# Optimization experiments

Hardware: AMD Instinct MI355X
Metric: run time of the kernel (lower is better)

## Reference

```python
import jax, jax.numpy as jnp
import numpy as np

MIN_STDDEV = 1e-05
STATE, ACTION, HIDDEN, RNN_H = 32, 8, 32, 32
B, T = 16384, 64


def setup_inputs() -> dict:
    key = jax.random.key(0)
    ks = jax.random.split(key, 16)
    sc = 0.1
    return {
        "s0": jax.random.normal(ks[0], (B, STATE), jnp.float32),
        "h0": jax.random.normal(ks[1], (1, B, RNN_H), jnp.float32),
        "actions": jax.random.normal(ks[2], (B, T, ACTION), jnp.float32),
        # Elman RNN params (PyTorch layout: W_ih [H, S+A], W_hh [H, H])
        "W_ih": jax.random.normal(ks[3], (RNN_H, STATE + ACTION), jnp.float32) * sc,
        "W_hh": jax.random.normal(ks[4], (RNN_H, RNN_H), jnp.float32) * sc,
        "b_ih": jax.random.normal(ks[5], (RNN_H,), jnp.float32) * sc,
        "b_hh": jax.random.normal(ks[6], (RNN_H,), jnp.float32) * sc,
        # Transition MLP: h -> elu(fc1) -> (mean, stddev)
        "fc1_w": jax.random.normal(ks[7], (HIDDEN, RNN_H), jnp.float32) * sc,
        "fc1_b": jax.random.normal(ks[8], (HIDDEN,), jnp.float32) * sc,
        "mean_w": jax.random.normal(ks[9], (STATE, HIDDEN), jnp.float32) * sc,
        "mean_b": jax.random.normal(ks[10], (STATE,), jnp.float32) * sc,
        "std_w": jax.random.normal(ks[11], (STATE, HIDDEN), jnp.float32) * sc,
        "std_b": jax.random.normal(ks[12], (STATE,), jnp.float32) * sc,
        "horizon_length": T,
    }


def reference(s0, h0, actions, W_ih, W_hh, b_ih, b_hh, fc1_w, fc1_b,
              mean_w, mean_b, std_w, std_b, horizon_length):
    # RSSM.rollout with mean_only=True: per step
    #   h_t = tanh(W_ih @ [s_{t-1}, a_{t-1}] + b_ih + W_hh @ h_{t-1} + b_hh)
    #   prior_t = Transition(h_t): mean, stddev = MLP(h_t); sample = mean
    n_steps = min(int(horizon_length), actions.shape[1])
    acts = jnp.transpose(actions[:, :n_steps], (1, 0, 2))  # [T, B, A]

    def step(carry, a):
        h, s = carry  # h: [B, H], s: [B, STATE] (prior sample = mean)
        x = jnp.concatenate([s, a], axis=-1)  # [B, STATE+A]
        h = jnp.tanh(x @ W_ih.T + b_ih + h @ W_hh.T + b_hh)
        hid = jax.nn.elu(h @ fc1_w.T + fc1_b)
        mean = hid @ mean_w.T + mean_b
        stddev = jax.nn.softplus(hid @ std_w.T + std_b) + MIN_STDDEV
        return (h, mean), (mean, stddev)

    (_, _), (means, stddevs) = jax.lax.scan(step, (h0[0], s0), acts)
    # pack prior means and stddevs: [T, B, 2*STATE]
    return jnp.concatenate([means, stddevs], axis=-1)
```

## Files before the change

### kernel.cpp

```cpp
#include <hip/hip_runtime.h>


#define NBATCH 16384
#define NSTEP  64
#define U_STRIDE 72
#define HID_STRIDE 40

typedef short bf16x8 __attribute__((ext_vector_type(8)));
typedef float f32x4  __attribute__((ext_vector_type(4)));

__device__ __forceinline__ short f2bf(float f) {
    union { float f; unsigned int u; } c; c.f = f;
    unsigned int r = c.u + 0x7fffu + ((c.u >> 16) & 1u);
    return (short)(r >> 16);
}

__global__ __launch_bounds__(64) void rssm_kernel(
    const float* __restrict__ s0, const float* __restrict__ h0,
    const float* __restrict__ actions,
    const float* __restrict__ W_ih, const float* __restrict__ W_hh,
    const float* __restrict__ b_ih, const float* __restrict__ b_hh,
    const float* __restrict__ fc1_w, const float* __restrict__ fc1_b,
    const float* __restrict__ mean_w, const float* __restrict__ mean_b,
    const float* __restrict__ std_w, const float* __restrict__ std_b,
    float* __restrict__ out)
{
    __shared__ alignas(16) short u_lds[16 * U_STRIDE];
    __shared__ alignas(16) short act_lds[NSTEP * 16 * 8];
    __shared__ alignas(16) short hid_lds[16 * HID_STRIDE];

    const int lane = threadIdx.x;
    const int n    = lane & 15;
    const int q    = lane >> 4;
    const int base = blockIdx.x * 16;

    bf16x8 wb[2][3], fw[2], mw[2], sw[2];
    #pragma unroll
    for (int hf = 0; hf < 2; ++hf) {
        const int col = hf * 16 + n;
        #pragma unroll
        for (int c = 0; c < 3; ++c)
            #pragma unroll
            for (int j = 0; j < 8; ++j) {
                const int kk = q * 8 + j;
                float w = 0.f;
                if (c == 0)              w = W_ih[col * 40 + kk];
                else if (c == 1)         w = W_hh[col * 32 + kk];
                else if (kk < 8)         w = W_ih[col * 40 + 32 + kk];
                wb[hf][c][j] = f2bf(w);
            }
        #pragma unroll
        for (int j = 0; j < 8; ++j) {
            const int k = q * 8 + j;
            fw[hf][j] = f2bf(fc1_w [col * 32 + k]);
            mw[hf][j] = f2bf(mean_w[col * 32 + k]);
            sw[hf][j] = f2bf(std_w [col * 32 + k]);
        }
    }
    float bc[2], fb[2], mb[2], sb[2];
    #pragma unroll
    for (int hf = 0; hf < 2; ++hf) {
        const int col = hf * 16 + n;
        bc[hf] = b_ih[col] + b_hh[col];
        fb[hf] = fc1_b[col];
        mb[hf] = mean_b[col];
        sb[hf] = std_b[col];
    }

    {
        const int m = lane >> 2;
        const int k = (lane & 3) * 8;
        bf16x8 sv, hv;
        #pragma unroll
        for (int j = 0; j < 8; ++j) {
            sv[j] = f2bf(s0[(size_t)(base + m) * 32 + k + j]);
            hv[j] = f2bf(h0[(size_t)(base + m) * 32 + k + j]);
        }
        *(bf16x8*)(&u_lds[m * U_STRIDE + k]) = sv;
        *(bf16x8*)(&u_lds[m * U_STRIDE + 32 + k]) = hv;
    }

    {
        const int arow = lane & 15;
        const int aq   = lane >> 4;
        const float* ap = actions + (size_t)(base + arow) * (NSTEP * 8);
        #pragma unroll
        for (int tt = 0; tt < 16; ++tt) {
            const int t = tt * 4 + aq;
            const f32x4 lo = *(const f32x4*)(ap + t * 8);
            const f32x4 hi = *(const f32x4*)(ap + t * 8 + 4);
            bf16x8 av;
            #pragma unroll
            for (int j = 0; j < 4; ++j) { av[j] = f2bf(lo[j]); av[4 + j] = f2bf(hi[j]); }
            *(bf16x8*)(&act_lds[(t * 16 + arow) * 8]) = av;
        }
    }
    __builtin_amdgcn_wave_barrier();

    float* outp[4];
    #pragma unroll
    for (int r = 0; r < 4; ++r)
        outp[r] = out + (size_t)(base + q * 4 + r) * 64 + n;

    const bf16x8 zfrag = {0, 0, 0, 0, 0, 0, 0, 0};

    for (int t = 0; t < NSTEP; ++t) {
        bf16x8 ua0 = *(const bf16x8*)(&u_lds[n * U_STRIDE + q * 8]);
        bf16x8 ua1 = *(const bf16x8*)(&u_lds[n * U_STRIDE + 32 + q * 8]);
        bf16x8 af  = zfrag;
        if (q == 0) af = *(const bf16x8*)(&act_lds[(t * 16 + n) * 8]);

        f32x4 acc0 = {bc[0], bc[0], bc[0], bc[0]};
        f32x4 acc1 = {bc[1], bc[1], bc[1], bc[1]};
        acc0 = __builtin_amdgcn_mfma_f32_16x16x32_bf16(ua0, wb[0][0], acc0, 0, 0, 0);
        acc0 = __builtin_amdgcn_mfma_f32_16x16x32_bf16(ua1, wb[0][1], acc0, 0, 0, 0);
        acc0 = __builtin_amdgcn_mfma_f32_16x16x32_bf16(af,  wb[0][2], acc0, 0, 0, 0);
        acc1 = __builtin_amdgcn_mfma_f32_16x16x32_bf16(ua0, wb[1][0], acc1, 0, 0, 0);
        acc1 = __builtin_amdgcn_mfma_f32_16x16x32_bf16(ua1, wb[1][1], acc1, 0, 0, 0);
        acc1 = __builtin_amdgcn_mfma_f32_16x16x32_bf16(af,  wb[1][2], acc1, 0, 0, 0);

        #pragma unroll
        for (int r = 0; r < 4; ++r) {
            const int m = q * 4 + r;
            float h0v = 1.f - 2.f / (__expf(2.f * acc0[r]) + 1.f);
            float h1v = 1.f - 2.f / (__expf(2.f * acc1[r]) + 1.f);
            u_lds[m * U_STRIDE + 32 + n]      = f2bf(h0v);
            u_lds[m * U_STRIDE + 32 + 16 + n] = f2bf(h1v);
        }
        __builtin_amdgcn_wave_barrier();

        bf16x8 ha = *(const bf16x8*)(&u_lds[n * U_STRIDE + 32 + q * 8]);
        f32x4 f0 = {fb[0], fb[0], fb[0], fb[0]};
        f32x4 f1 = {fb[1], fb[1], fb[1], fb[1]};
        f0 = __builtin_amdgcn_mfma_f32_16x16x32_bf16(ha, fw[0], f0, 0, 0, 0);
        f1 = __builtin_amdgcn_mfma_f32_16x16x32_bf16(ha, fw[1], f1, 0, 0, 0);

        #pragma unroll
        for (int r = 0; r < 4; ++r) {
            const int m = q * 4 + r;
            float x0 = f0[r], x1 = f1[r];
            float e0 = x0 > 0.f ? x0 : (__expf(x0) - 1.f);
            float e1 = x1 > 0.f ? x1 : (__expf(x1) - 1.f);
            hid_lds[m * HID_STRIDE + n]      = f2bf(e0);
            hid_lds[m * HID_STRIDE + 16 + n] = f2bf(e1);
        }
        __builtin_amdgcn_wave_barrier();

        bf16x8 da = *(const bf16x8*)(&hid_lds[n * HID_STRIDE + q * 8]);
        f32x4 m0 = {mb[0], mb[0], mb[0], mb[0]};
        f32x4 m1 = {mb[1], mb[1], mb[1], mb[1]};
        f32x4 v0 = {sb[0], sb[0], sb[0], sb[0]};
        f32x4 v1 = {sb[1], sb[1], sb[1], sb[1]};
        m0 = __builtin_amdgcn_mfma_f32_16x16x32_bf16(da, mw[0], m0, 0, 0, 0);
        m1 = __builtin_amdgcn_mfma_f32_16x16x32_bf16(da, mw[1], m1, 0, 0, 0);
        v0 = __builtin_amdgcn_mfma_f32_16x16x32_bf16(da, sw[0], v0, 0, 0, 0);
        v1 = __builtin_amdgcn_mfma_f32_16x16x32_bf16(da, sw[1], v1, 0, 0, 0);

        #pragma unroll
        for (int r = 0; r < 4; ++r) {
            const int m = q * 4 + r;
            u_lds[m * U_STRIDE + n]      = f2bf(m0[r]);
            u_lds[m * U_STRIDE + 16 + n] = f2bf(m1[r]);
        }
        __builtin_amdgcn_wave_barrier();

        #pragma unroll
        for (int r = 0; r < 4; ++r) {
            float x0 = v0[r], x1 = v1[r];
            float sp0 = fmaxf(x0, 0.f) + __logf(1.f + __expf(-fabsf(x0)));
            float sp1 = fmaxf(x1, 0.f) + __logf(1.f + __expf(-fabsf(x1)));
            float* p = outp[r];
            p[0]  = m0[r];
            p[16] = m1[r];
            p[32] = sp0 + 1e-5f;
            p[48] = sp1 + 1e-5f;
            outp[r] += (size_t)NBATCH * 64;
        }
    }
}

extern "C" void kernel_launch(void* const* d_in, const int* in_sizes, int n_in,
                              void* d_out, int out_size, void* d_ws, size_t ws_size,
                              hipStream_t stream) {
    (void)in_sizes; (void)n_in; (void)out_size; (void)d_ws; (void)ws_size;
    rssm_kernel<<<dim3(NBATCH / 16), dim3(64), 0, stream>>>(
        (const float*)d_in[0],  (const float*)d_in[1],  (const float*)d_in[2],
        (const float*)d_in[3],  (const float*)d_in[4],  (const float*)d_in[5],
        (const float*)d_in[6],  (const float*)d_in[7],  (const float*)d_in[8],
        (const float*)d_in[9],  (const float*)d_in[10], (const float*)d_in[11],
        (const float*)d_in[12], (float*)d_out);
}
```

Before: 353.9 us.

## Shrink batch rows per wave to four and pack two waves per block

Each wave now handles 4 batch rows instead of 16, padding the MFMA M dimension with zero rows, and each block holds two independent waves. This turns 1024 waves into 4096 so the latency-bound serial recurrence is spread across many more waves and CUs. The cost is that three quarters of each MFMA's rows do wasted work and total instruction count rises about fourfold.

Measured after the change: 467.0 us. +32.0%, slower.

```diff
diff --git a/kernel.cpp b/kernel.cpp
--- a/kernel.cpp
+++ b/kernel.cpp
@@ -3,10 +3,12 @@
 
 #define NBATCH 16384
 #define NSTEP  64
+#define ROWS   4
 #define U_STRIDE 72
 #define HID_STRIDE 40
 
 typedef short bf16x8 __attribute__((ext_vector_type(8)));
+typedef short bf16x4 __attribute__((ext_vector_type(4)));
 typedef float f32x4  __attribute__((ext_vector_type(4)));
 
 __device__ __forceinline__ short f2bf(float f) {
@@ -15,7 +17,7 @@
     return (short)(r >> 16);
 }
 
-__global__ __launch_bounds__(64) void rssm_kernel(
+__global__ __launch_bounds__(128, 4) void rssm_kernel(
     const float* __restrict__ s0, const float* __restrict__ h0,
     const float* __restrict__ actions,
     const float* __restrict__ W_ih, const float* __restrict__ W_hh,
@@ -25,14 +27,20 @@
     const float* __restrict__ std_w, const float* __restrict__ std_b,
     float* __restrict__ out)
 {
-    __shared__ alignas(16) short u_lds[16 * U_STRIDE];
-    __shared__ alignas(16) short act_lds[NSTEP * 16 * 8];
-    __shared__ alignas(16) short hid_lds[16 * HID_STRIDE];
+    __shared__ alignas(16) short u_lds[2][16 * U_STRIDE];
+    __shared__ alignas(16) short act_lds[2][NSTEP * ROWS * 8];
+    __shared__ alignas(16) short hid_lds[2][16 * HID_STRIDE];
 
-    const int lane = threadIdx.x;
+    const int tid  = threadIdx.x;
+    const int wid  = tid >> 6;
+    const int lane = tid & 63;
     const int n    = lane & 15;
     const int q    = lane >> 4;
-    const int base = blockIdx.x * 16;
+    const int base = (blockIdx.x * 2 + wid) * ROWS;
+
+    short* __restrict__ u   = u_lds[wid];
+    short* __restrict__ act = act_lds[wid];
+    short* __restrict__ hid = hid_lds[wid];
 
     bf16x8 wb[2][3], fw[2], mw[2], sw[2];
     #pragma unroll
@@ -67,48 +75,44 @@
         sb[hf] = std_b[col];
     }
 
+    for (int i = lane; i < 16 * U_STRIDE; i += 64) u[i] = 0;
+    __builtin_amdgcn_wave_barrier();
+
     {
-        const int m = lane >> 2;
-        const int k = (lane & 3) * 8;
-        bf16x8 sv, hv;
-        #pragma unroll
-        for (int j = 0; j < 8; ++j) {
-            sv[j] = f2bf(s0[(size_t)(base + m) * 32 + k + j]);
-            hv[j] = f2bf(h0[(size_t)(base + m) * 32 + k + j]);
-        }
-        *(bf16x8*)(&u_lds[m * U_STRIDE + k]) = sv;
-        *(bf16x8*)(&u_lds[m * U_STRIDE + 32 + k]) = hv;
+        const int row = lane >> 4;
+        const int c2  = (lane & 15) * 2;
+        const size_t rb = (size_t)(base + row) * 32 + c2;
+        u[row * U_STRIDE + c2]          = f2bf(s0[rb]);
+        u[row * U_STRIDE + c2 + 1]      = f2bf(s0[rb + 1]);
+        u[row * U_STRIDE + 32 + c2]     = f2bf(h0[rb]);
+        u[row * U_STRIDE + 32 + c2 + 1] = f2bf(h0[rb + 1]);
     }
 
-    {
-        const int arow = lane & 15;
-        const int aq   = lane >> 4;
-        const float* ap = actions + (size_t)(base + arow) * (NSTEP * 8);
+    #pragma unroll
+    for (int it = 0; it < 8; ++it) {
+        const int flat = it * 64 + lane;
+        const int row  = flat >> 7;
+        const int rem  = flat & 127;
+        const int t    = rem >> 1;
+        const int half = rem & 1;
+        const f32x4 a4 = *(const f32x4*)(actions
+            + (size_t)(base + row) * (NSTEP * 8) + t * 8 + half * 4);
+        bf16x4 av;
         #pragma unroll
-        for (int tt = 0; tt < 16; ++tt) {
-            const int t = tt * 4 + aq;
-            const f32x4 lo = *(const f32x4*)(ap + t * 8);
-            const f32x4 hi = *(const f32x4*)(ap + t * 8 + 4);
-            bf16x8 av;
-            #pragma unroll
-            for (int j = 0; j < 4; ++j) { av[j] = f2bf(lo[j]); av[4 + j] = f2bf(hi[j]); }
-            *(bf16x8*)(&act_lds[(t * 16 + arow) * 8]) = av;
-        }
+        for (int j = 0; j < 4; ++j) av[j] = f2bf(a4[j]);
+        *(bf16x4*)(&act[(t * ROWS + row) * 8 + half * 4]) = av;
     }
     __builtin_amdgcn_wave_barrier();
 
-    float* outp[4];
-    #pragma unroll
-    for (int r = 0; r < 4; ++r)
-        outp[r] = out + (size_t)(base + q * 4 + r) * 64 + n;
+    float* op = out + (size_t)base * 64 + n;
 
     const bf16x8 zfrag = {0, 0, 0, 0, 0, 0, 0, 0};
 
     for (int t = 0; t < NSTEP; ++t) {
-        bf16x8 ua0 = *(const bf16x8*)(&u_lds[n * U_STRIDE + q * 8]);
-        bf16x8 ua1 = *(const bf16x8*)(&u_lds[n * U_STRIDE + 32 + q * 8]);
+        bf16x8 ua0 = *(const bf16x8*)(&u[n * U_STRIDE + q * 8]);
+        bf16x8 ua1 = *(const bf16x8*)(&u[n * U_STRIDE + 32 + q * 8]);
         bf16x8 af  = zfrag;
-        if (q == 0) af = *(const bf16x8*)(&act_lds[(t * 16 + n) * 8]);
+        if (q == 0 && n < ROWS) af = *(const bf16x8*)(&act[(t * ROWS + n) * 8]);
 
         f32x4 acc0 = {bc[0], bc[0], bc[0], bc[0]};
         f32x4 acc1 = {bc[1], bc[1], bc[1], bc[1]};
@@ -124,12 +128,12 @@
             const int m = q * 4 + r;
             float h0v = 1.f - 2.f / (__expf(2.f * acc0[r]) + 1.f);
             float h1v = 1.f - 2.f / (__expf(2.f * acc1[r]) + 1.f);
-            u_lds[m * U_STRIDE + 32 + n]      = f2bf(h0v);
-            u_lds[m * U_STRIDE + 32 + 16 + n] = f2bf(h1v);
+            u[m * U_STRIDE + 32 + n]      = f2bf(h0v);
+            u[m * U_STRIDE + 32 + 16 + n] = f2bf(h1v);
         }
         __builtin_amdgcn_wave_barrier();
 
-        bf16x8 ha = *(const bf16x8*)(&u_lds[n * U_STRIDE + 32 + q * 8]);
+        bf16x8 ha = *(const bf16x8*)(&u[n * U_STRIDE + 32 + q * 8]);
         f32x4 f0 = {fb[0], fb[0], fb[0], fb[0]};
         f32x4 f1 = {fb[1], fb[1], fb[1], fb[1]};
         f0 = __builtin_amdgcn_mfma_f32_16x16x32_bf16(ha, fw[0], f0, 0, 0, 0);
@@ -141,12 +145,12 @@
             float x0 = f0[r], x1 = f1[r];
             float e0 = x0 > 0.f ? x0 : (__expf(x0) - 1.f);
             float e1 = x1 > 0.f ? x1 : (__expf(x1) - 1.f);
-            hid_lds[m * HID_STRIDE + n]      = f2bf(e0);
-            hid_lds[m * HID_STRIDE + 16 + n] = f2bf(e1);
+            hid[m * HID_STRIDE + n]      = f2bf(e0);
+            hid[m * HID_STRIDE + 16 + n] = f2bf(e1);
         }
         __builtin_amdgcn_wave_barrier();
 
-        bf16x8 da = *(const bf16x8*)(&hid_lds[n * HID_STRIDE + q * 8]);
+        bf16x8 da = *(const bf16x8*)(&hid[n * HID_STRIDE + q * 8]);
         f32x4 m0 = {mb[0], mb[0], mb[0], mb[0]};
         f32x4 m1 = {mb[1], mb[1], mb[1], mb[1]};
         f32x4 v0 = {sb[0], sb[0], sb[0], sb[0]};
@@ -159,23 +163,24 @@
         #pragma unroll
         for (int r = 0; r < 4; ++r) {
             const int m = q * 4 + r;
-            u_lds[m * U_STRIDE + n]      = f2bf(m0[r]);
-            u_lds[m * U_STRIDE + 16 + n] = f2bf(m1[r]);
+            u[m * U_STRIDE + n]      = f2bf(m0[r]);
+            u[m * U_STRIDE + 16 + n] = f2bf(m1[r]);
         }
         __builtin_amdgcn_wave_barrier();
 
-        #pragma unroll
-        for (int r = 0; r < 4; ++r) {
-            float x0 = v0[r], x1 = v1[r];
-            float sp0 = fmaxf(x0, 0.f) + __logf(1.f + __expf(-fabsf(x0)));
-            float sp1 = fmaxf(x1, 0.f) + __logf(1.f + __expf(-fabsf(x1)));
-            float* p = outp[r];
-            p[0]  = m0[r];
-            p[16] = m1[r];
-            p[32] = sp0 + 1e-5f;
-            p[48] = sp1 + 1e-5f;
-            outp[r] += (size_t)NBATCH * 64;
+        if (q == 0) {
+            #pragma unroll
+            for (int r = 0; r < 4; ++r) {
+                float x0 = v0[r], x1 = v1[r];
+                float sp0 = fmaxf(x0, 0.f) + __logf(1.f + __expf(-fabsf(x0)));
+                float sp1 = fmaxf(x1, 0.f) + __logf(1.f + __expf(-fabsf(x1)));
+                op[r * 64]      = m0[r];
+                op[r * 64 + 16] = m1[r];
+                op[r * 64 + 32] = sp0 + 1e-5f;
+                op[r * 64 + 48] = sp1 + 1e-5f;
+            }
         }
+        op += (size_t)NBATCH * 64;
     }
 }
 
@@ -183,7 +188,7 @@
                               void* d_out, int out_size, void* d_ws, size_t ws_size,
                               hipStream_t stream) {
     (void)in_sizes; (void)n_in; (void)out_size; (void)d_ws; (void)ws_size;
-    rssm_kernel<<<dim3(NBATCH / 16), dim3(64), 0, stream>>>(
+    rssm_kernel<<<dim3(NBATCH / (2 * ROWS)), dim3(128), 0, stream>>>(
         (const float*)d_in[0],  (const float*)d_in[1],  (const float*)d_in[2],
         (const float*)d_in[3],  (const float*)d_in[4],  (const float*)d_in[5],
         (const float*)d_in[6],  (const float*)d_in[7],  (const float*)d_in[8],
```
